# Optimization experiments

Hardware: AMD Instinct MI355X
Metric: run time of the kernel (lower is better)

The kernel has to match this reference:

```python
import jax, jax.numpy as jnp
import numpy as np
import math

B, S, D, H = 2, 2048, 2048, 16
DH = D // H
NEG = -1e9  # finite stand-in for -inf so fully-masked rows stay NaN-free


def setup_inputs() -> dict:
    key = jax.random.key(0)
    ks = jax.random.split(key, 6)
    x = jax.random.normal(ks[0], (B, S, D), dtype=jnp.float32)
    key_padding_mask = jax.random.randint(ks[1], (B, S), 0, 2, dtype=jnp.int32)
    Wqkv_w = jax.random.normal(ks[2], (3 * D, D), dtype=jnp.float32) / math.sqrt(D)
    Wqkv_b = jnp.zeros((3 * D,), dtype=jnp.float32)
    out_w = jax.random.normal(ks[3], (D, D), dtype=jnp.float32) / math.sqrt(D)
    out_b = jnp.zeros((D,), dtype=jnp.float32)
    return {"x": x, "key_padding_mask": key_padding_mask, "Wqkv_w": Wqkv_w,
            "Wqkv_b": Wqkv_b, "out_w": out_w, "out_b": out_b}


def reference(x, key_padding_mask, Wqkv_w, Wqkv_b, out_w, out_b):
    b, s, d = x.shape
    # fused QKV projection (torch Linear: y = x @ W.T + b)
    qkv = (x @ Wqkv_w.T + Wqkv_b).reshape(b, s, 3, H, DH)
    q, k, v = qkv[:, :, 0], qkv[:, :, 1], qkv[:, :, 2]  # each [b, s, H, DH]
    scale = 1.0 / math.sqrt(DH)
    scores = jnp.einsum('bqhd,bkhd->bhqk', q, k) * scale  # [b, H, s, s]
    # additive key-padding bias: -inf where mask == 0 (finite NEG for stability)
    pad_bias = jnp.where(key_padding_mask == 0, NEG, 0.0).astype(x.dtype)[:, None, None, :]
    # causal mask: key index > query index is disallowed
    causal = jnp.where(jnp.arange(s)[None, :] > jnp.arange(s)[:, None], NEG, 0.0).astype(x.dtype)
    p = jax.nn.softmax(scores + pad_bias + causal, axis=-1)
    attn = jnp.einsum('bhqk,bkhd->bqhd', p, v).reshape(b, s, d)
    return attn @ out_w.T + out_b
```

## Files before the change

### kernel.cpp

```cpp
#include <hip/hip_runtime.h>
#include <cstdint>

typedef unsigned short u16;
typedef __attribute__((ext_vector_type(8))) short short8v;
typedef __attribute__((ext_vector_type(8))) unsigned short u16x8;
typedef __attribute__((ext_vector_type(4))) float floatx4;

typedef unsigned int __attribute__((address_space(1))) as1_u32;
typedef unsigned int __attribute__((address_space(3))) as3_u32;

__device__ __forceinline__ u16 f2bf(float f) {
  union { float f; unsigned u; } v; v.f = f;
  unsigned r = v.u + 0x7FFFu + ((v.u >> 16) & 1u);
  return (u16)(r >> 16);
}

__device__ __forceinline__ unsigned cvt_pk_bf16(float lo, float hi) {
  unsigned r;
  asm("v_cvt_pk_bf16_f32 %0, %1, %2" : "=v"(r) : "v"(lo), "v"(hi));
  return r;
}

__device__ __forceinline__ void gload16(void* lds, const void* g) {
  __builtin_amdgcn_global_load_lds((as1_u32*)(uintptr_t)g, (as3_u32*)(uintptr_t)lds, 16, 0, 0);
}

__global__ __launch_bounds__(256) void f2bf_kernel(const float* __restrict__ in,
                                                   u16* __restrict__ out, int n4) {
  int i = blockIdx.x * 256 + threadIdx.x;
  const int stride = gridDim.x * 256;
  for (; i < n4; i += stride) {
    float4 v = ((const float4*)in)[i];
    ushort4 o;
    o.x = f2bf(v.x); o.y = f2bf(v.y); o.z = f2bf(v.z); o.w = f2bf(v.w);
    ((ushort4*)out)[i] = o;
  }
}

template <int OUT_BF16>
__global__ __launch_bounds__(512, 4)
void gemm_v4(const u16* __restrict__ A, const u16* __restrict__ B,
             const float* __restrict__ bias, void* __restrict__ C,
             int M, int N, int K) {
  __shared__ u16 Al[3][4096];
  __shared__ u16 Bl[3][8192];
  const int tid = threadIdx.x;
  const int wid = tid >> 6, lane = tid & 63;
  const int wr = wid >> 2, wc = wid & 3;
  const int li = lane & 15, lg = lane >> 4;
  const int nwg = gridDim.x;
  const int bid = blockIdx.x;
  const int swz = (bid & 7) * (nwg >> 3) + (bid >> 3);
  const int mcnt = M >> 7;
  const int bm = swz % mcnt, bn = swz / mcnt;
  const int brow = bm * 128, bcol = bn * 256;
  const int NT = K >> 5;

  const int P = tid * 16;
  const int pr = P >> 7;
  const int innerLog = (P & 127) ^ ((pr & 7) << 4);
  const int srow = (pr << 1) + (innerLog >> 6);
  const int skb = innerLog & 63;
  const u16* aS = A + (size_t)(brow + srow) * K + (skb >> 1);
  const u16* bS = B + (size_t)(bcol + srow) * K + (skb >> 1);

#define STG(slot, kt_)                                                          \
  {                                                                             \
    const u16* a_ = aS + (kt_) * 32;                                            \
    const u16* b_ = bS + (kt_) * 32;                                            \
    gload16((char*)&Al[slot][0] + P, a_);                                       \
    gload16((char*)&Bl[slot][0] + P, b_);                                       \
    gload16((char*)&Bl[slot][0] + 8192 + P, b_ + (size_t)128 * K);              \
  }

  floatx4 acc[4][4];
#pragma unroll
  for (int m = 0; m < 4; ++m)
#pragma unroll
    for (int n = 0; n < 4; ++n) acc[m][n] = floatx4{0.f, 0.f, 0.f, 0.f};

  const int fxor = ((li >> 1) & 7) << 4;
  const int finner = (((li & 1) << 6) + (lg << 4)) ^ fxor;
  const int aoff = (wr * 32 + (li >> 1)) * 128 + finner;
  const int boff = (wc * 32 + (li >> 1)) * 128 + finner;

  STG(0, 0);
  STG(1, 1);
  asm volatile("s_waitcnt vmcnt(3)" ::: "memory");
  __builtin_amdgcn_s_barrier();

  int sl = 0;
  for (int t = 0; t < NT; ++t) {
    const char* Ab = (const char*)&Al[sl][0];
    const char* Bb = (const char*)&Bl[sl][0];
    short8v af[4], bf[4];
#pragma unroll
    for (int m = 0; m < 4; ++m) af[m] = *(const short8v*)(Ab + aoff + m * 1024);
#pragma unroll
    for (int n = 0; n < 4; ++n) bf[n] = *(const short8v*)(Bb + boff + n * 1024);

    int s2 = sl + 2; if (s2 >= 3) s2 -= 3;
    if (t + 2 < NT) STG(s2, t + 2);

    __builtin_amdgcn_s_setprio(1);
#pragma unroll
    for (int m = 0; m < 4; ++m)
#pragma unroll
      for (int n = 0; n < 4; ++n)
        acc[m][n] = __builtin_amdgcn_mfma_f32_16x16x32_bf16(af[m], bf[n], acc[m][n], 0, 0, 0);
    __builtin_amdgcn_s_setprio(0);

    if (t + 2 < NT)      asm volatile("s_waitcnt vmcnt(3)" ::: "memory");
    else if (t + 1 < NT) asm volatile("s_waitcnt vmcnt(0)" ::: "memory");
    __builtin_amdgcn_s_barrier();
    sl = (sl + 1 == 3) ? 0 : sl + 1;
  }
#undef STG

  const int crow0 = brow + wr * 64 + lg * 4;
  const int ccol0 = bcol + wc * 64 + li;
#pragma unroll
  for (int n = 0; n < 4; ++n) {
    const float bv = bias[ccol0 + n * 16];
#pragma unroll
    for (int m = 0; m < 4; ++m) {
#pragma unroll
      for (int j = 0; j < 4; ++j) {
        const float v = acc[m][n][j] + bv;
        const size_t idx = (size_t)(crow0 + m * 16 + j) * N + (ccol0 + n * 16);
        if (OUT_BF16) ((u16*)C)[idx] = f2bf(v);
        else          ((float*)C)[idx] = v;
      }
    }
  }
}

__global__ __launch_bounds__(256)
void transpose_v(const u16* __restrict__ qkv, u16* __restrict__ vt) {
  __shared__ u16 T[64][136];
  const int st = blockIdx.x, bh = blockIdx.y;
  const int b = bh >> 4, h = bh & 15;
  const int tid = threadIdx.x;
  const u16* src = qkv + (size_t)(b * 2048 + st * 64) * 6144 + 4096 + h * 128;
  u16* dst = vt + (size_t)bh * 128 * 2048 + st * 64;
#pragma unroll
  for (int p = 0; p < 4; ++p) {
    const int e = (p * 256 + tid) * 8;
    const int r = e >> 7, c = e & 127;
    *(u16x8*)&T[r][c] = *(const u16x8*)&src[(size_t)r * 6144 + c];
  }
  __syncthreads();
#pragma unroll
  for (int p = 0; p < 4; ++p) {
    const int e = (p * 256 + tid) * 8;
    const int dh = e >> 6, s0 = e & 63;
    u16x8 o;
#pragma unroll
    for (int j = 0; j < 8; ++j) o[j] = T[s0 + j][dh];
    *(u16x8*)&dst[(size_t)dh * 2048 + s0] = o;
  }
}

__global__ __launch_bounds__(256, 2)
void attn_fused(const u16* __restrict__ qkv, const u16* __restrict__ vt,
                const int* __restrict__ kpm, u16* __restrict__ attn_out) {
  constexpr int S = 2048, DQ = 6144;
  __shared__ u16 Kl[2][64 * 128];
  __shared__ u16 Vl[128 * 64];
  __shared__ float mskf[2048];
  __shared__ int s_any;
  const int bx = blockIdx.x, by = blockIdx.y;
  const int qt = ((by >> 4) & 1) ? bx : (15 - bx);
  const int bh = by;
  const int b = bh >> 4, h = bh & 15;
  const int tid = threadIdx.x, wave = tid >> 6, lane = tid & 63;
  const int lg = lane >> 4, li = lane & 15;
  const int qrow0 = qt * 128 + wave * 32;

  const u16* Qb = qkv + (size_t)b * S * DQ + h * 128;
  const u16* Kb = Qb + 2048;
  const u16* Vtb = vt + (size_t)bh * 128 * 2048;
  const int* mrow = kpm + b * S;

  if (tid == 0) s_any = 0;
  __syncthreads();
  {
    int a = 0;
    for (int j = tid; j < 2048; j += 256) {
      const int mv = mrow[j];
      mskf[j] = mv ? 0.f : -1.0e9f;
      if (mv && j <= qt * 128) a = 1;
    }
    if (a) s_any = 1;
  }
  __syncthreads();
  const int anyv = s_any;
  const int nt = anyv ? (2 * qt + 2) : 32;
  const int causalFromW = anyv ? (qrow0 >> 6) : 0;

  short8v qb[2][4];
#pragma unroll
  for (int m = 0; m < 2; ++m) {
    const u16* qp = Qb + (size_t)(qrow0 + m * 16 + li) * DQ + lg * 8;
#pragma unroll
    for (int kk = 0; kk < 4; ++kk) qb[m][kk] = *(const short8v*)(qp + kk * 32);
  }
  asm volatile("s_waitcnt vmcnt(0)" ::: "memory");

  float mM[2], lSum[2];
  floatx4 oa[2][8];
#pragma unroll
  for (int m = 0; m < 2; ++m) {
    mM[m] = -3.0e38f; lSum[m] = 0.f;
#pragma unroll
    for (int n = 0; n < 8; ++n) oa[m][n] = floatx4{0.f, 0.f, 0.f, 0.f};
  }

  const u16* kSrc[4]; const u16* vSrc[4];
#pragma unroll
  for (int i = 0; i < 4; ++i) {
    const int L = i * 4096 + tid * 16;
    const int r = L >> 8;
    const int c = ((L & 255) ^ ((r & 7) << 4)) >> 1;
    kSrc[i] = Kb + (size_t)r * DQ + c;
    const int d = L >> 7;
    const int sv = ((L & 127) ^ ((d & 7) << 4)) >> 1;
    vSrc[i] = Vtb + (size_t)d * 2048 + sv;
  }

#define STAGE_K(buf, kt_)                                                      \
  {                                                                            \
    const int kv0_ = (kt_) * 64;                                               \
    _Pragma("unroll")                                                          \
    for (int i = 0; i < 4; ++i)                                                \
      gload16((char*)Kl + (buf) * 16384 + i * 4096 + tid * 16,                 \
              kSrc[i] + (size_t)kv0_ * DQ);                                    \
  }
#define STAGE_V(kt_)                                                           \
  {                                                                            \
    const int kv0_ = (kt_) * 64;                                               \
    _Pragma("unroll")                                                          \
    for (int i = 0; i < 4; ++i)                                                \
      gload16((char*)Vl + i * 4096 + tid * 16, vSrc[i] + kv0_);                \
  }

  const float scale = 0.08838834764831845f;

  STAGE_K(0, 0);
  STAGE_V(0);

  for (int kt = 0; kt < nt; ++kt) {
    const int cur = kt & 1;
    const int kv0 = kt * 64;
    if (kt + 1 < nt) {
      STAGE_K(cur ^ 1, kt + 1);
      asm volatile("s_waitcnt vmcnt(8)" ::: "memory");
    } else {
      asm volatile("s_waitcnt vmcnt(4)" ::: "memory");
    }
    __builtin_amdgcn_s_barrier();

    const char* Kcur = (const char*)Kl + cur * 16384;

    floatx4 sc[2][4];
#pragma unroll
    for (int n = 0; n < 4; ++n) { sc[0][n] = floatx4{0,0,0,0}; sc[1][n] = floatx4{0,0,0,0}; }
#pragma unroll
    for (int n = 0; n < 4; ++n) {
      const int r = n * 16 + li;
#pragma unroll
      for (int kk = 0; kk < 4; ++kk) {
        const int byteo = (r * 256 + kk * 64 + lg * 16) ^ ((r & 7) << 4);
        const short8v kf = *(const short8v*)(Kcur + byteo);
        sc[0][n] = __builtin_amdgcn_mfma_f32_16x16x32_bf16(kf, qb[0][kk], sc[0][n], 0, 0, 0);
        sc[1][n] = __builtin_amdgcn_mfma_f32_16x16x32_bf16(kf, qb[1][kk], sc[1][n], 0, 0, 0);
      }
    }

    floatx4 pbv[4];
#pragma unroll
    for (int n = 0; n < 4; ++n)
      pbv[n] = *(const floatx4*)&mskf[kv0 + n * 16 + lg * 4];
    const bool cz = (kt >= causalFromW);

    short8v pf[2][2];
#pragma unroll
    for (int m = 0; m < 2; ++m) {
      const int q_l = qrow0 + m * 16 + li;
      float tmax = -3.0e38f;
#pragma unroll
      for (int n = 0; n < 4; ++n)
#pragma unroll
        for (int j = 0; j < 4; ++j) {
          float s = sc[m][n][j] * scale + pbv[n][j];
          if (cz && (kv0 + n * 16 + lg * 4 + j > q_l)) s -= 1.0e9f;
          sc[m][n][j] = s;
          tmax = fmaxf(tmax, s);
        }
      tmax = fmaxf(tmax, __shfl_xor(tmax, 16));
      tmax = fmaxf(tmax, __shfl_xor(tmax, 32));
      const float mnew = fmaxf(mM[m], tmax);
      const float f = __expf(mM[m] - mnew);
      mM[m] = mnew;
      float rs = 0.f;
#pragma unroll
      for (int n = 0; n < 4; ++n)
#pragma unroll
        for (int j = 0; j < 4; ++j) {
          const float e = __expf(sc[m][n][j] - mnew);
          sc[m][n][j] = e; rs += e;
        }
      rs += __shfl_xor(rs, 16);
      rs += __shfl_xor(rs, 32);
      lSum[m] = lSum[m] * f + rs;
#pragma unroll
      for (int n2 = 0; n2 < 8; ++n2) oa[m][n2] *= f;

      unsigned w32[4][2];
#pragma unroll
      for (int n = 0; n < 4; ++n) {
        w32[n][0] = cvt_pk_bf16(sc[m][n][0], sc[m][n][1]);
        w32[n][1] = cvt_pk_bf16(sc[m][n][2], sc[m][n][3]);
      }
      union PF { short8v s; unsigned w[4]; } pfu[2];
#pragma unroll
      for (int kk2 = 0; kk2 < 2; ++kk2) {
#pragma unroll
        for (int hh = 0; hh < 2; ++hh) {
          unsigned u = w32[2 * kk2][hh], v = w32[2 * kk2 + 1][hh];
          asm volatile("v_permlane32_swap_b32 %0, %1" : "+v"(u), "+v"(v));
          asm volatile("v_permlane16_swap_b32 %0, %1" : "+v"(u), "+v"(v));
          pfu[kk2].w[hh] = u;
          pfu[kk2].w[2 + hh] = v;
        }
      }
      pf[m][0] = pfu[0].s;
      pf[m][1] = pfu[1].s;
    }

    if (kt + 1 < nt) asm volatile("s_waitcnt vmcnt(4)" ::: "memory");
    else             asm volatile("s_waitcnt vmcnt(0)" ::: "memory");
    __builtin_amdgcn_s_barrier();

#pragma unroll
    for (int kk2 = 0; kk2 < 2; ++kk2) {
#pragma unroll
      for (int n2 = 0; n2 < 8; ++n2) {
        const int d = n2 * 16 + li;
        const int vbyte = (d * 128 + kk2 * 64 + lg * 16) ^ ((d & 7) << 4);
        const short8v vf = *(const short8v*)((const char*)Vl + vbyte);
        oa[0][n2] = __builtin_amdgcn_mfma_f32_16x16x32_bf16(vf, pf[0][kk2], oa[0][n2], 0, 0, 0);
        oa[1][n2] = __builtin_amdgcn_mfma_f32_16x16x32_bf16(vf, pf[1][kk2], oa[1][n2], 0, 0, 0);
      }
    }
    __builtin_amdgcn_s_barrier();
    if (kt + 1 < nt) STAGE_V(kt + 1);
  }

  {
    char* Ol = (char*)Kl + wave * 8192;
#pragma unroll
    for (int m = 0; m < 2; ++m) {
      const float inv = 1.0f / lSum[m];
      const int q_ = m * 16 + li;
#pragma unroll
      for (int n2 = 0; n2 < 8; ++n2) {
        unsigned lo = cvt_pk_bf16(oa[m][n2][0] * inv, oa[m][n2][1] * inv);
        unsigned hi = cvt_pk_bf16(oa[m][n2][2] * inv, oa[m][n2][3] * inv);
        const int byteo = (q_ * 256 + n2 * 32 + lg * 8) ^ ((q_ & 7) << 4);
        uint2 pr2; pr2.x = lo; pr2.y = hi;
        *(uint2*)(Ol + byteo) = pr2;
      }
    }
    asm volatile("s_waitcnt lgkmcnt(0)" ::: "memory");
#pragma unroll
    for (int rr = 0; rr < 4; ++rr) {
      const int r = rr * 8 + (lane >> 3);
      const size_t grow = (size_t)(b * 2048 + qt * 128 + wave * 32 + r) * 2048 + h * 128;
#pragma unroll
      for (int s2 = 0; s2 < 2; ++s2) {
        const int byteo = (r * 256 + (lane & 7) * 32 + s2 * 16) ^ ((r & 7) << 4);
        const u16x8 val = *(const u16x8*)(Ol + byteo);
        *(u16x8*)&attn_out[grow + (lane & 7) * 16 + s2 * 8] = val;
      }
    }
  }
#undef STAGE_K
#undef STAGE_V
}

extern "C" void kernel_launch(void* const* d_in, const int* in_sizes, int n_in,
                              void* d_out, int out_size, void* d_ws, size_t ws_size,
                              hipStream_t stream) {
  const float* x    = (const float*)d_in[0];
  const int*   kpm  = (const int*)d_in[1];
  const float* wqkv = (const float*)d_in[2];
  const float* bqkv = (const float*)d_in[3];
  const float* wout = (const float*)d_in[4];
  const float* bout = (const float*)d_in[5];
  float* out = (float*)d_out;

  char* ws = (char*)d_ws;
  u16* xbf   = (u16*)(ws);
  u16* wqbf  = (u16*)(ws + (16u << 20));
  u16* wobf  = (u16*)(ws + (40u << 20));
  u16* qkvb  = (u16*)(ws + (48u << 20));
  u16* vtb   = (u16*)(ws + (96u << 20));
  u16* attnb = (u16*)(ws + (112u << 20));

  f2bf_kernel<<<1024, 256, 0, stream>>>(x,    xbf,  4096 * 2048 / 4);
  f2bf_kernel<<<1024, 256, 0, stream>>>(wqkv, wqbf, 6144 * 2048 / 4);
  f2bf_kernel<<<1024, 256, 0, stream>>>(wout, wobf, 2048 * 2048 / 4);

  gemm_v4<1><<<768, 512, 0, stream>>>(xbf, wqbf, bqkv, qkvb, 4096, 6144, 2048);
  transpose_v<<<dim3(32, 32), 256, 0, stream>>>(qkvb, vtb);
  attn_fused<<<dim3(16, 32), 256, 0, stream>>>(qkvb, vtb, kpm, attnb);
  gemm_v4<0><<<256, 512, 0, stream>>>(attnb, wobf, bout, out, 4096, 2048, 2048);
}
```

Before: 286.2 us.

## Use 8 waves per attention block and a triple-buffered 128x128 output GEMM

The attention kernel now runs 512 threads per block, each wave owning 16 query rows instead of 32. This halves per-wave register state and lets more waves hide the softmax and memory latency. The key-padding mask is stored in shared memory as u16 flags instead of float biases. The output projection moves to a new 128x128-tile GEMM with a triple-buffered LDS pipeline, 256 threads and s_setprio around the MFMAs, giving 512 blocks instead of 256. The trade-off is more barrier traffic per KV tile in attention and less reuse per wave.

```diff
diff --git a/kernel.cpp b/kernel.cpp
--- a/kernel.cpp
+++ b/kernel.cpp
@@ -135,6 +135,105 @@
   }
 }
 
+template <int OUT_BF16>
+__global__ __launch_bounds__(256, 4)
+void gemm_s(const u16* __restrict__ A, const u16* __restrict__ B,
+            const float* __restrict__ bias, void* __restrict__ C,
+            int M, int N, int K) {
+  __shared__ u16 Al[3][4096];
+  __shared__ u16 Bl[3][4096];
+  const int tid = threadIdx.x;
+  const int wid = tid >> 6, lane = tid & 63;
+  const int wr = wid >> 1, wc = wid & 1;
+  const int li = lane & 15, lg = lane >> 4;
+  const int nwg = gridDim.x;
+  const int bid = blockIdx.x;
+  const int swz = (bid & 7) * (nwg >> 3) + (bid >> 3);
+  const int mcnt = M >> 7;
+  const int bm = swz % mcnt, bn = swz / mcnt;
+  const int brow = bm * 128, bcol = bn * 128;
+  const int NT = K >> 5;
+
+  const int P = tid * 16;
+  const int pr = P >> 7;
+  const int innerLog = (P & 127) ^ ((pr & 7) << 4);
+  const int srow = (pr << 1) + (innerLog >> 6);
+  const int skb = innerLog & 63;
+  const u16* aS = A + (size_t)(brow + srow) * K + (skb >> 1);
+  const u16* bS = B + (size_t)(bcol + srow) * K + (skb >> 1);
+
+#define STG(slot, kt_)                                                          \
+  {                                                                             \
+    const u16* a_ = aS + (kt_) * 32;                                            \
+    const u16* b_ = bS + (kt_) * 32;                                            \
+    gload16((char*)&Al[slot][0] + P, a_);                                       \
+    gload16((char*)&Al[slot][0] + 4096 + P, a_ + (size_t)64 * K);               \
+    gload16((char*)&Bl[slot][0] + P, b_);                                       \
+    gload16((char*)&Bl[slot][0] + 4096 + P, b_ + (size_t)64 * K);               \
+  }
+
+  floatx4 acc[4][4];
+#pragma unroll
+  for (int m = 0; m < 4; ++m)
+#pragma unroll
+    for (int n = 0; n < 4; ++n) acc[m][n] = floatx4{0.f, 0.f, 0.f, 0.f};
+
+  const int fxor = ((li >> 1) & 7) << 4;
+  const int finner = (((li & 1) << 6) + (lg << 4)) ^ fxor;
+  const int aoff = (wr * 32 + (li >> 1)) * 128 + finner;
+  const int boff = (wc * 32 + (li >> 1)) * 128 + finner;
+
+  STG(0, 0);
+  STG(1, 1);
+  asm volatile("s_waitcnt vmcnt(4)" ::: "memory");
+  __builtin_amdgcn_s_barrier();
+
+  int sl = 0;
+  for (int t = 0; t < NT; ++t) {
+    const char* Ab = (const char*)&Al[sl][0];
+    const char* Bb = (const char*)&Bl[sl][0];
+    short8v af[4], bf[4];
+#pragma unroll
+    for (int m = 0; m < 4; ++m) af[m] = *(const short8v*)(Ab + aoff + m * 1024);
+#pragma unroll
+    for (int n = 0; n < 4; ++n) bf[n] = *(const short8v*)(Bb + boff + n * 1024);
+
+    int s2 = sl + 2; if (s2 >= 3) s2 -= 3;
+    if (t + 2 < NT) STG(s2, t + 2);
+
+    __builtin_amdgcn_s_setprio(1);
+#pragma unroll
+    for (int m = 0; m < 4; ++m)
+#pragma unroll
+      for (int n = 0; n < 4; ++n)
+        acc[m][n] = __builtin_amdgcn_mfma_f32_16x16x32_bf16(af[m], bf[n], acc[m][n], 0, 0, 0);
+    __builtin_amdgcn_s_setprio(0);
+
+    if (t + 2 < NT)      asm volatile("s_waitcnt vmcnt(4)" ::: "memory");
+    else if (t + 1 < NT) asm volatile("s_waitcnt vmcnt(0)" ::: "memory");
+    __builtin_amdgcn_s_barrier();
+    sl = (sl + 1 == 3) ? 0 : sl + 1;
+  }
+#undef STG
+
+  const int crow0 = brow + wr * 64 + lg * 4;
+  const int ccol0 = bcol + wc * 64 + li;
+#pragma unroll
+  for (int n = 0; n < 4; ++n) {
+    const float bv = bias[ccol0 + n * 16];
+#pragma unroll
+    for (int m = 0; m < 4; ++m) {
+#pragma unroll
+      for (int j = 0; j < 4; ++j) {
+        const float v = acc[m][n][j] + bv;
+        const size_t idx = (size_t)(crow0 + m * 16 + j) * N + (ccol0 + n * 16);
+        if (OUT_BF16) ((u16*)C)[idx] = f2bf(v);
+        else          ((float*)C)[idx] = v;
+      }
+    }
+  }
+}
+
 __global__ __launch_bounds__(256)
 void transpose_v(const u16* __restrict__ qkv, u16* __restrict__ vt) {
   __shared__ u16 T[64][136];
@@ -161,13 +260,13 @@
   }
 }
 
-__global__ __launch_bounds__(256, 2)
+__global__ __launch_bounds__(512, 2)
 void attn_fused(const u16* __restrict__ qkv, const u16* __restrict__ vt,
                 const int* __restrict__ kpm, u16* __restrict__ attn_out) {
   constexpr int S = 2048, DQ = 6144;
   __shared__ u16 Kl[2][64 * 128];
   __shared__ u16 Vl[128 * 64];
-  __shared__ float mskf[2048];
+  __shared__ u16 msk[2048];
   __shared__ int s_any;
   const int bx = blockIdx.x, by = blockIdx.y;
   const int qt = ((by >> 4) & 1) ? bx : (15 - bx);
@@ -175,7 +274,7 @@
   const int b = bh >> 4, h = bh & 15;
   const int tid = threadIdx.x, wave = tid >> 6, lane = tid & 63;
   const int lg = lane >> 4, li = lane & 15;
-  const int qrow0 = qt * 128 + wave * 32;
+  const int qrow0 = qt * 128 + wave * 16;
 
   const u16* Qb = qkv + (size_t)b * S * DQ + h * 128;
   const u16* Kb = Qb + 2048;
@@ -186,9 +285,9 @@
   __syncthreads();
   {
     int a = 0;
-    for (int j = tid; j < 2048; j += 256) {
+    for (int j = tid; j < 2048; j += 512) {
       const int mv = mrow[j];
-      mskf[j] = mv ? 0.f : -1.0e9f;
+      msk[j] = (u16)(mv != 0);
       if (mv && j <= qt * 128) a = 1;
     }
     if (a) s_any = 1;
@@ -198,28 +297,23 @@
   const int nt = anyv ? (2 * qt + 2) : 32;
   const int causalFromW = anyv ? (qrow0 >> 6) : 0;
 
-  short8v qb[2][4];
-#pragma unroll
-  for (int m = 0; m < 2; ++m) {
-    const u16* qp = Qb + (size_t)(qrow0 + m * 16 + li) * DQ + lg * 8;
-#pragma unroll
-    for (int kk = 0; kk < 4; ++kk) qb[m][kk] = *(const short8v*)(qp + kk * 32);
+  short8v qb[4];
+  {
+    const u16* qp = Qb + (size_t)(qrow0 + li) * DQ + lg * 8;
+#pragma unroll
+    for (int kk = 0; kk < 4; ++kk) qb[kk] = *(const short8v*)(qp + kk * 32);
   }
   asm volatile("s_waitcnt vmcnt(0)" ::: "memory");
 
-  float mM[2], lSum[2];
-  floatx4 oa[2][8];
-#pragma unroll
-  for (int m = 0; m < 2; ++m) {
-    mM[m] = -3.0e38f; lSum[m] = 0.f;
-#pragma unroll
-    for (int n = 0; n < 8; ++n) oa[m][n] = floatx4{0.f, 0.f, 0.f, 0.f};
-  }
-
-  const u16* kSrc[4]; const u16* vSrc[4];
-#pragma unroll
-  for (int i = 0; i < 4; ++i) {
-    const int L = i * 4096 + tid * 16;
+  float mM = -3.0e38f, lSum = 0.f;
+  floatx4 oa[8];
+#pragma unroll
+  for (int n = 0; n < 8; ++n) oa[n] = floatx4{0.f, 0.f, 0.f, 0.f};
+
+  const u16* kSrc[2]; const u16* vSrc[2];
+#pragma unroll
+  for (int i = 0; i < 2; ++i) {
+    const int L = i * 8192 + tid * 16;
     const int r = L >> 8;
     const int c = ((L & 255) ^ ((r & 7) << 4)) >> 1;
     kSrc[i] = Kb + (size_t)r * DQ + c;
@@ -232,16 +326,16 @@
   {                                                                            \
     const int kv0_ = (kt_) * 64;                                               \
     _Pragma("unroll")                                                          \
-    for (int i = 0; i < 4; ++i)                                                \
-      gload16((char*)Kl + (buf) * 16384 + i * 4096 + tid * 16,                 \
+    for (int i = 0; i < 2; ++i)                                                \
+      gload16((char*)Kl + (buf) * 16384 + i * 8192 + tid * 16,                 \
               kSrc[i] + (size_t)kv0_ * DQ);                                    \
   }
 #define STAGE_V(kt_)                                                           \
   {                                                                            \
     const int kv0_ = (kt_) * 64;                                               \
     _Pragma("unroll")                                                          \
-    for (int i = 0; i < 4; ++i)                                                \
-      gload16((char*)Vl + i * 4096 + tid * 16, vSrc[i] + kv0_);                \
+    for (int i = 0; i < 2; ++i)                                                \
+      gload16((char*)Vl + i * 8192 + tid * 16, vSrc[i] + kv0_);                \
   }
 
   const float scale = 0.08838834764831845f;
@@ -254,17 +348,17 @@
     const int kv0 = kt * 64;
     if (kt + 1 < nt) {
       STAGE_K(cur ^ 1, kt + 1);
-      asm volatile("s_waitcnt vmcnt(8)" ::: "memory");
+      asm volatile("s_waitcnt vmcnt(4)" ::: "memory");
     } else {
-      asm volatile("s_waitcnt vmcnt(4)" ::: "memory");
+      asm volatile("s_waitcnt vmcnt(2)" ::: "memory");
     }
     __builtin_amdgcn_s_barrier();
 
     const char* Kcur = (const char*)Kl + cur * 16384;
 
-    floatx4 sc[2][4];
-#pragma unroll
-    for (int n = 0; n < 4; ++n) { sc[0][n] = floatx4{0,0,0,0}; sc[1][n] = floatx4{0,0,0,0}; }
+    floatx4 sc[4];
+#pragma unroll
+    for (int n = 0; n < 4; ++n) sc[n] = floatx4{0.f, 0.f, 0.f, 0.f};
 #pragma unroll
     for (int n = 0; n < 4; ++n) {
       const int r = n * 16 + li;
@@ -272,55 +366,55 @@
       for (int kk = 0; kk < 4; ++kk) {
         const int byteo = (r * 256 + kk * 64 + lg * 16) ^ ((r & 7) << 4);
         const short8v kf = *(const short8v*)(Kcur + byteo);
-        sc[0][n] = __builtin_amdgcn_mfma_f32_16x16x32_bf16(kf, qb[0][kk], sc[0][n], 0, 0, 0);
-        sc[1][n] = __builtin_amdgcn_mfma_f32_16x16x32_bf16(kf, qb[1][kk], sc[1][n], 0, 0, 0);
-      }
-    }
-
-    floatx4 pbv[4];
+        sc[n] = __builtin_amdgcn_mfma_f32_16x16x32_bf16(kf, qb[kk], sc[n], 0, 0, 0);
+      }
+    }
+
+    ushort4 mfl[4];
 #pragma unroll
     for (int n = 0; n < 4; ++n)
-      pbv[n] = *(const floatx4*)&mskf[kv0 + n * 16 + lg * 4];
+      mfl[n] = *(const ushort4*)&msk[kv0 + n * 16 + lg * 4];
     const bool cz = (kt >= causalFromW);
 
-    short8v pf[2][2];
-#pragma unroll
-    for (int m = 0; m < 2; ++m) {
-      const int q_l = qrow0 + m * 16 + li;
-      float tmax = -3.0e38f;
-#pragma unroll
-      for (int n = 0; n < 4; ++n)
-#pragma unroll
-        for (int j = 0; j < 4; ++j) {
-          float s = sc[m][n][j] * scale + pbv[n][j];
-          if (cz && (kv0 + n * 16 + lg * 4 + j > q_l)) s -= 1.0e9f;
-          sc[m][n][j] = s;
-          tmax = fmaxf(tmax, s);
-        }
-      tmax = fmaxf(tmax, __shfl_xor(tmax, 16));
-      tmax = fmaxf(tmax, __shfl_xor(tmax, 32));
-      const float mnew = fmaxf(mM[m], tmax);
-      const float f = __expf(mM[m] - mnew);
-      mM[m] = mnew;
-      float rs = 0.f;
-#pragma unroll
-      for (int n = 0; n < 4; ++n)
-#pragma unroll
-        for (int j = 0; j < 4; ++j) {
-          const float e = __expf(sc[m][n][j] - mnew);
-          sc[m][n][j] = e; rs += e;
-        }
-      rs += __shfl_xor(rs, 16);
-      rs += __shfl_xor(rs, 32);
-      lSum[m] = lSum[m] * f + rs;
-#pragma unroll
-      for (int n2 = 0; n2 < 8; ++n2) oa[m][n2] *= f;
-
+    const int q_l = qrow0 + li;
+    float tmax = -3.0e38f;
+#pragma unroll
+    for (int n = 0; n < 4; ++n) {
+      const u16 fl[4] = {mfl[n].x, mfl[n].y, mfl[n].z, mfl[n].w};
+#pragma unroll
+      for (int j = 0; j < 4; ++j) {
+        float s = sc[n][j] * scale + (fl[j] ? 0.f : -1.0e9f);
+        if (cz && (kv0 + n * 16 + lg * 4 + j > q_l)) s -= 1.0e9f;
+        sc[n][j] = s;
+        tmax = fmaxf(tmax, s);
+      }
+    }
+    tmax = fmaxf(tmax, __shfl_xor(tmax, 16));
+    tmax = fmaxf(tmax, __shfl_xor(tmax, 32));
+    const float mnew = fmaxf(mM, tmax);
+    const float f = __expf(mM - mnew);
+    mM = mnew;
+    float rs = 0.f;
+#pragma unroll
+    for (int n = 0; n < 4; ++n)
+#pragma unroll
+      for (int j = 0; j < 4; ++j) {
+        const float e = __expf(sc[n][j] - mnew);
+        sc[n][j] = e; rs += e;
+      }
+    rs += __shfl_xor(rs, 16);
+    rs += __shfl_xor(rs, 32);
+    lSum = lSum * f + rs;
+#pragma unroll
+    for (int n2 = 0; n2 < 8; ++n2) oa[n2] *= f;
+
+    short8v pf[2];
+    {
       unsigned w32[4][2];
 #pragma unroll
       for (int n = 0; n < 4; ++n) {
-        w32[n][0] = cvt_pk_bf16(sc[m][n][0], sc[m][n][1]);
-        w32[n][1] = cvt_pk_bf16(sc[m][n][2], sc[m][n][3]);
+        w32[n][0] = cvt_pk_bf16(sc[n][0], sc[n][1]);
+        w32[n][1] = cvt_pk_bf16(sc[n][2], sc[n][3]);
       }
       union PF { short8v s; unsigned w[4]; } pfu[2];
 #pragma unroll
@@ -334,11 +428,11 @@
           pfu[kk2].w[2 + hh] = v;
         }
       }
-      pf[m][0] = pfu[0].s;
-      pf[m][1] = pfu[1].s;
-    }
-
-    if (kt + 1 < nt) asm volatile("s_waitcnt vmcnt(4)" ::: "memory");
+      pf[0] = pfu[0].s;
+      pf[1] = pfu[1].s;
+    }
+
+    if (kt + 1 < nt) asm volatile("s_waitcnt vmcnt(2)" ::: "memory");
     else             asm volatile("s_waitcnt vmcnt(0)" ::: "memory");
     __builtin_amdgcn_s_barrier();
 
@@ -349,8 +443,7 @@
         const int d = n2 * 16 + li;
         const int vbyte = (d * 128 + kk2 * 64 + lg * 16) ^ ((d & 7) << 4);
         const short8v vf = *(const short8v*)((const char*)Vl + vbyte);
-        oa[0][n2] = __builtin_amdgcn_mfma_f32_16x16x32_bf16(vf, pf[0][kk2], oa[0][n2], 0, 0, 0);
-        oa[1][n2] = __builtin_amdgcn_mfma_f32_16x16x32_bf16(vf, pf[1][kk2], oa[1][n2], 0, 0, 0);
+        oa[n2] = __builtin_amdgcn_mfma_f32_16x16x32_bf16(vf, pf[kk2], oa[n2], 0, 0, 0);
       }
     }
     __builtin_amdgcn_s_barrier();
@@ -358,31 +451,24 @@
   }
 
   {
-    char* Ol = (char*)Kl + wave * 8192;
-#pragma unroll
-    for (int m = 0; m < 2; ++m) {
-      const float inv = 1.0f / lSum[m];
-      const int q_ = m * 16 + li;
-#pragma unroll
-      for (int n2 = 0; n2 < 8; ++n2) {
-        unsigned lo = cvt_pk_bf16(oa[m][n2][0] * inv, oa[m][n2][1] * inv);
-        unsigned hi = cvt_pk_bf16(oa[m][n2][2] * inv, oa[m][n2][3] * inv);
-        const int byteo = (q_ * 256 + n2 * 32 + lg * 8) ^ ((q_ & 7) << 4);
-        uint2 pr2; pr2.x = lo; pr2.y = hi;
-        *(uint2*)(Ol + byteo) = pr2;
-      }
+    char* Ol = (char*)Kl + wave * 4096;
+    const float inv = 1.0f / lSum;
+#pragma unroll
+    for (int n2 = 0; n2 < 8; ++n2) {
+      unsigned lo = cvt_pk_bf16(oa[n2][0] * inv, oa[n2][1] * inv);
+      unsigned hi = cvt_pk_bf16(oa[n2][2] * inv, oa[n2][3] * inv);
+      const int byteo = (li * 256 + n2 * 32 + lg * 8) ^ ((li & 7) << 4);
+      uint2 pr2; pr2.x = lo; pr2.y = hi;
+      *(uint2*)(Ol + byteo) = pr2;
     }
     asm volatile("s_waitcnt lgkmcnt(0)" ::: "memory");
 #pragma unroll
     for (int rr = 0; rr < 4; ++rr) {
-      const int r = rr * 8 + (lane >> 3);
-      const size_t grow = (size_t)(b * 2048 + qt * 128 + wave * 32 + r) * 2048 + h * 128;
-#pragma unroll
-      for (int s2 = 0; s2 < 2; ++s2) {
-        const int byteo = (r * 256 + (lane & 7) * 32 + s2 * 16) ^ ((r & 7) << 4);
-        const u16x8 val = *(const u16x8*)(Ol + byteo);
-        *(u16x8*)&attn_out[grow + (lane & 7) * 16 + s2 * 8] = val;
-      }
+      const int r = rr * 4 + lg;
+      const size_t grow = (size_t)(b * 2048 + qrow0 + r) * 2048 + h * 128;
+      const int byteo = (r * 256 + li * 16) ^ ((r & 7) << 4);
+      const u16x8 val = *(const u16x8*)(Ol + byteo);
+      *(u16x8*)&attn_out[grow + li * 8] = val;
     }
   }
 #undef STAGE_K
@@ -414,6 +500,6 @@
 
   gemm_v4<1><<<768, 512, 0, stream>>>(xbf, wqbf, bqkv, qkvb, 4096, 6144, 2048);
   transpose_v<<<dim3(32, 32), 256, 0, stream>>>(qkvb, vtb);
-  attn_fused<<<dim3(16, 32), 256, 0, stream>>>(qkvb, vtb, kpm, attnb);
-  gemm_v4<0><<<256, 512, 0, stream>>>(attnb, wobf, bout, out, 4096, 2048, 2048);
-}
+  attn_fused<<<dim3(16, 32), 512, 0, stream>>>(qkvb, vtb, kpm, attnb);
+  gemm_s<0><<<512, 256, 0, stream>>>(attnb, wobf, bout, out, 4096, 2048, 2048);
+}
```

Measured after the change: 323.2 us. +12.9%, slower.

## Load V fragments directly from global memory and add triple-buffered output GEMM

Applied to the files above, without the earlier changes.

In the attention kernel, the LDS staging of transposed V tiles is removed. Each wave now reads its V MFMA fragments straight from global memory, which drops one barrier and a wait per KV tile and frees LDS. The output projection switches to a new 128x128-tile, 256-thread GEMM with a three-slot LDS ring buffer and a swizzled block order, launched with 512 blocks. The risks are uncoalesced and redundant global V reads across the four waves of a block, and the different occupancy of the new GEMM.

```diff
diff --git a/kernel.cpp b/kernel.cpp
--- a/kernel.cpp
+++ b/kernel.cpp
@@ -135,6 +135,105 @@
   }
 }
 
+template <int OUT_BF16>
+__global__ __launch_bounds__(256, 4)
+void gemm_s(const u16* __restrict__ A, const u16* __restrict__ B,
+            const float* __restrict__ bias, void* __restrict__ C,
+            int M, int N, int K) {
+  __shared__ u16 Al[3][4096];
+  __shared__ u16 Bl[3][4096];
+  const int tid = threadIdx.x;
+  const int wid = tid >> 6, lane = tid & 63;
+  const int wr = wid >> 1, wc = wid & 1;
+  const int li = lane & 15, lg = lane >> 4;
+  const int nwg = gridDim.x;
+  const int bid = blockIdx.x;
+  const int swz = (bid & 7) * (nwg >> 3) + (bid >> 3);
+  const int mcnt = M >> 7;
+  const int bm = swz % mcnt, bn = swz / mcnt;
+  const int brow = bm * 128, bcol = bn * 128;
+  const int NT = K >> 5;
+
+  const int P = tid * 16;
+  const int pr = P >> 7;
+  const int innerLog = (P & 127) ^ ((pr & 7) << 4);
+  const int srow = (pr << 1) + (innerLog >> 6);
+  const int skb = innerLog & 63;
+  const u16* aS = A + (size_t)(brow + srow) * K + (skb >> 1);
+  const u16* bS = B + (size_t)(bcol + srow) * K + (skb >> 1);
+
+#define STG(slot, kt_)                                                          \
+  {                                                                             \
+    const u16* a_ = aS + (kt_) * 32;                                            \
+    const u16* b_ = bS + (kt_) * 32;                                            \
+    gload16((char*)&Al[slot][0] + P, a_);                                       \
+    gload16((char*)&Al[slot][0] + 4096 + P, a_ + (size_t)64 * K);               \
+    gload16((char*)&Bl[slot][0] + P, b_);                                       \
+    gload16((char*)&Bl[slot][0] + 4096 + P, b_ + (size_t)64 * K);               \
+  }
+
+  floatx4 acc[4][4];
+#pragma unroll
+  for (int m = 0; m < 4; ++m)
+#pragma unroll
+    for (int n = 0; n < 4; ++n) acc[m][n] = floatx4{0.f, 0.f, 0.f, 0.f};
+
+  const int fxor = ((li >> 1) & 7) << 4;
+  const int finner = (((li & 1) << 6) + (lg << 4)) ^ fxor;
+  const int aoff = (wr * 32 + (li >> 1)) * 128 + finner;
+  const int boff = (wc * 32 + (li >> 1)) * 128 + finner;
+
+  STG(0, 0);
+  STG(1, 1);
+  asm volatile("s_waitcnt vmcnt(4)" ::: "memory");
+  __builtin_amdgcn_s_barrier();
+
+  int sl = 0;
+  for (int t = 0; t < NT; ++t) {
+    const char* Ab = (const char*)&Al[sl][0];
+    const char* Bb = (const char*)&Bl[sl][0];
+    short8v af[4], bf[4];
+#pragma unroll
+    for (int m = 0; m < 4; ++m) af[m] = *(const short8v*)(Ab + aoff + m * 1024);
+#pragma unroll
+    for (int n = 0; n < 4; ++n) bf[n] = *(const short8v*)(Bb + boff + n * 1024);
+
+    int s2 = sl + 2; if (s2 >= 3) s2 -= 3;
+    if (t + 2 < NT) STG(s2, t + 2);
+
+    __builtin_amdgcn_s_setprio(1);
+#pragma unroll
+    for (int m = 0; m < 4; ++m)
+#pragma unroll
+      for (int n = 0; n < 4; ++n)
+        acc[m][n] = __builtin_amdgcn_mfma_f32_16x16x32_bf16(af[m], bf[n], acc[m][n], 0, 0, 0);
+    __builtin_amdgcn_s_setprio(0);
+
+    if (t + 2 < NT)      asm volatile("s_waitcnt vmcnt(4)" ::: "memory");
+    else if (t + 1 < NT) asm volatile("s_waitcnt vmcnt(0)" ::: "memory");
+    __builtin_amdgcn_s_barrier();
+    sl = (sl + 1 == 3) ? 0 : sl + 1;
+  }
+#undef STG
+
+  const int crow0 = brow + wr * 64 + lg * 4;
+  const int ccol0 = bcol + wc * 64 + li;
+#pragma unroll
+  for (int n = 0; n < 4; ++n) {
+    const float bv = bias[ccol0 + n * 16];
+#pragma unroll
+    for (int m = 0; m < 4; ++m) {
+#pragma unroll
+      for (int j = 0; j < 4; ++j) {
+        const float v = acc[m][n][j] + bv;
+        const size_t idx = (size_t)(crow0 + m * 16 + j) * N + (ccol0 + n * 16);
+        if (OUT_BF16) ((u16*)C)[idx] = f2bf(v);
+        else          ((float*)C)[idx] = v;
+      }
+    }
+  }
+}
+
 __global__ __launch_bounds__(256)
 void transpose_v(const u16* __restrict__ qkv, u16* __restrict__ vt) {
   __shared__ u16 T[64][136];
@@ -166,7 +265,6 @@
                 const int* __restrict__ kpm, u16* __restrict__ attn_out) {
   constexpr int S = 2048, DQ = 6144;
   __shared__ u16 Kl[2][64 * 128];
-  __shared__ u16 Vl[128 * 64];
   __shared__ float mskf[2048];
   __shared__ int s_any;
   const int bx = blockIdx.x, by = blockIdx.y;
@@ -216,17 +314,15 @@
     for (int n = 0; n < 8; ++n) oa[m][n] = floatx4{0.f, 0.f, 0.f, 0.f};
   }
 
-  const u16* kSrc[4]; const u16* vSrc[4];
+  const u16* kSrc[4];
 #pragma unroll
   for (int i = 0; i < 4; ++i) {
     const int L = i * 4096 + tid * 16;
     const int r = L >> 8;
     const int c = ((L & 255) ^ ((r & 7) << 4)) >> 1;
     kSrc[i] = Kb + (size_t)r * DQ + c;
-    const int d = L >> 7;
-    const int sv = ((L & 127) ^ ((d & 7) << 4)) >> 1;
-    vSrc[i] = Vtb + (size_t)d * 2048 + sv;
-  }
+  }
+  const u16* vBase = Vtb + (size_t)li * 2048 + lg * 8;
 
 #define STAGE_K(buf, kt_)                                                      \
   {                                                                            \
@@ -236,27 +332,19 @@
       gload16((char*)Kl + (buf) * 16384 + i * 4096 + tid * 16,                 \
               kSrc[i] + (size_t)kv0_ * DQ);                                    \
   }
-#define STAGE_V(kt_)                                                           \
-  {                                                                            \
-    const int kv0_ = (kt_) * 64;                                               \
-    _Pragma("unroll")                                                          \
-    for (int i = 0; i < 4; ++i)                                                \
-      gload16((char*)Vl + i * 4096 + tid * 16, vSrc[i] + kv0_);                \
-  }
 
   const float scale = 0.08838834764831845f;
 
   STAGE_K(0, 0);
-  STAGE_V(0);
 
   for (int kt = 0; kt < nt; ++kt) {
     const int cur = kt & 1;
     const int kv0 = kt * 64;
     if (kt + 1 < nt) {
       STAGE_K(cur ^ 1, kt + 1);
-      asm volatile("s_waitcnt vmcnt(8)" ::: "memory");
+      asm volatile("s_waitcnt vmcnt(4)" ::: "memory");
     } else {
-      asm volatile("s_waitcnt vmcnt(4)" ::: "memory");
+      asm volatile("s_waitcnt vmcnt(0)" ::: "memory");
     }
     __builtin_amdgcn_s_barrier();
 
@@ -338,23 +426,16 @@
       pf[m][1] = pfu[1].s;
     }
 
-    if (kt + 1 < nt) asm volatile("s_waitcnt vmcnt(4)" ::: "memory");
-    else             asm volatile("s_waitcnt vmcnt(0)" ::: "memory");
-    __builtin_amdgcn_s_barrier();
-
 #pragma unroll
     for (int kk2 = 0; kk2 < 2; ++kk2) {
 #pragma unroll
       for (int n2 = 0; n2 < 8; ++n2) {
-        const int d = n2 * 16 + li;
-        const int vbyte = (d * 128 + kk2 * 64 + lg * 16) ^ ((d & 7) << 4);
-        const short8v vf = *(const short8v*)((const char*)Vl + vbyte);
+        const short8v vf = *(const short8v*)(vBase + (size_t)(n2 * 16) * 2048 + kv0 + kk2 * 32);
         oa[0][n2] = __builtin_amdgcn_mfma_f32_16x16x32_bf16(vf, pf[0][kk2], oa[0][n2], 0, 0, 0);
         oa[1][n2] = __builtin_amdgcn_mfma_f32_16x16x32_bf16(vf, pf[1][kk2], oa[1][n2], 0, 0, 0);
       }
     }
     __builtin_amdgcn_s_barrier();
-    if (kt + 1 < nt) STAGE_V(kt + 1);
   }
 
   {
@@ -386,7 +467,6 @@
     }
   }
 #undef STAGE_K
-#undef STAGE_V
 }
 
 extern "C" void kernel_launch(void* const* d_in, const int* in_sizes, int n_in,
@@ -415,5 +495,5 @@
   gemm_v4<1><<<768, 512, 0, stream>>>(xbf, wqbf, bqkv, qkvb, 4096, 6144, 2048);
   transpose_v<<<dim3(32, 32), 256, 0, stream>>>(qkvb, vtb);
   attn_fused<<<dim3(16, 32), 256, 0, stream>>>(qkvb, vtb, kpm, attnb);
-  gemm_v4<0><<<256, 512, 0, stream>>>(attnb, wobf, bout, out, 4096, 2048, 2048);
-}
+  gemm_s<0><<<512, 256, 0, stream>>>(attnb, wobf, bout, out, 4096, 2048, 2048);
+}
```

After: 353.7 us. 23.6% more time.
